# Kernel optimization log

Hardware: AMD Instinct MI355X
Metric: run time of the kernel (lower is better)

Reference implementation:

```python
import jax, jax.numpy as jnp
import numpy as np

D_MODEL = 512
NUM_HEADS = 8
WINDOW = 64
HEAD_DIM = D_MODEL // NUM_HEADS


def setup_inputs() -> dict:
    key = jax.random.key(0)
    k1, k2, k3 = jax.random.split(key, 3)
    B, F, L, D = 4, 16, 2048, D_MODEL
    x = jax.random.normal(k1, (B, F, L, D), dtype=jnp.float32)
    w_qkv = jax.random.normal(k2, (D, 3 * D), dtype=jnp.float32) * (1.0 / np.sqrt(D))
    b_qkv = jnp.zeros((3 * D,), dtype=jnp.float32)
    w_proj = jax.random.normal(k3, (D, D), dtype=jnp.float32) * (1.0 / np.sqrt(D))
    b_proj = jnp.zeros((D,), dtype=jnp.float32)
    return {"x": x, "w_qkv": w_qkv, "b_qkv": b_qkv, "w_proj": w_proj, "b_proj": b_proj}


def reference(x, w_qkv, b_qkv, w_proj, b_proj):
    B, F, L, D = x.shape
    W = WINDOW
    H, hd = NUM_HEADS, HEAD_DIM
    nw = L // W  # L chosen divisible by window_size; pad path is identity here
    # partition into windows: (B, F, nw, W, D)
    xw = x.reshape(B, F, nw, W, D)
    # fused QKV projection
    qkv = jnp.einsum('bfnwd,de->bfnwe', xw, w_qkv) + b_qkv  # (B,F,nw,W,3D)
    qkv = qkv.reshape(B, F, nw, W, 3, H, hd)
    q = qkv[..., 0, :, :]  # (B,F,nw,W,H,hd)
    k = qkv[..., 1, :, :]
    v = qkv[..., 2, :, :]
    scale = 1.0 / np.sqrt(hd).astype(np.float32)
    # per-window attention: scores (B,F,nw,H,W,W)
    scores = jnp.einsum('bfnqhd,bfnkhd->bfnhqk', q, k) * scale
    attn = jax.nn.softmax(scores, axis=-1)
    out = jnp.einsum('bfnhqk,bfnkhd->bfnqhd', attn, v)  # (B,F,nw,W,H,hd)
    out = out.reshape(B, F, nw, W, D)
    out = jnp.einsum('bfnwd,de->bfnwe', out, w_proj) + b_proj
    return out.reshape(B, F, L, D)
```

## Files before the change

### kernel.cpp

```cpp
#include <hip/hip_runtime.h>

typedef __attribute__((ext_vector_type(8))) short short8;
typedef __attribute__((ext_vector_type(4))) float f32x4;
typedef unsigned short u16;
typedef unsigned int u32;

__device__ __forceinline__ u16 f2bf(float f){
  union { float f; u32 u; } v; v.f = f;
  u32 u = v.u;
  u32 r = (u + 0x7FFFu + ((u >> 16) & 1u)) >> 16;
  return (u16)r;
}

__device__ __forceinline__ u32 cvtpk(float a, float b){
  u32 r;
  asm("v_cvt_pk_bf16_f32 %0, %1, %2" : "=v"(r) : "v"(a), "v"(b));
  return r;
}

__device__ __forceinline__ int swz(int row, int cb){ return cb ^ ((row & 7) << 4); }

__device__ __forceinline__ void gload16(const void* g, void* l){
  __builtin_amdgcn_global_load_lds(
      (const __attribute__((address_space(1))) unsigned int*)g,
      (__attribute__((address_space(3))) unsigned int*)l, 16, 0, 0);
}

__global__ void convert_weights_swz(const float* __restrict__ wqkv,
                                    const float* __restrict__ wproj,
                                    u16* __restrict__ wq_swz,
                                    u16* __restrict__ wpt){
  int c = blockIdx.x * 256 + threadIdx.x;
  union { u16 u[8]; uint4 v; } t;
  if (c < 98304){
    int tile = c >> 10, row = (c >> 3) & 127, c7 = c & 7;
    int bn = tile >> 3, kt = tile & 7;
    int j  = c7 ^ (row & 7);
    int e  = bn * 128 + row;
    int k0 = kt * 64 + j * 8;
    #pragma unroll
    for (int i = 0; i < 8; ++i) t.u[i] = f2bf(wqkv[(long)(k0 + i) * 1536 + e]);
    *reinterpret_cast<uint4*>(wq_swz + (long)c * 8) = t.v;
  } else {
    int t2 = c - 98304;
    int cc = t2 >> 6;
    int kc = (t2 & 63) << 3;
    #pragma unroll
    for (int i = 0; i < 8; ++i) t.u[i] = f2bf(wproj[(long)(kc + i) * 512 + cc]);
    *reinterpret_cast<uint4*>(wpt + (long)cc * 512 + kc) = t.v;
  }
}

__global__ void convert_x(const float* __restrict__ x, u16* __restrict__ xbf){
  int c = blockIdx.x * 256 + threadIdx.x;
  int tile = c >> 10, row = (c >> 3) & 127, c7 = c & 7;
  int bm = tile >> 3, kt = tile & 7;
  int j  = c7 ^ (row & 7);
  const float* src = x + (long)(bm * 128 + row) * 512 + kt * 64 + j * 8;
  float4 v0 = *reinterpret_cast<const float4*>(src);
  float4 v1 = *reinterpret_cast<const float4*>(src + 4);
  union { u16 u[8]; uint4 v; } t;
  t.u[0] = f2bf(v0.x); t.u[1] = f2bf(v0.y); t.u[2] = f2bf(v0.z); t.u[3] = f2bf(v0.w);
  t.u[4] = f2bf(v1.x); t.u[5] = f2bf(v1.y); t.u[6] = f2bf(v1.z); t.u[7] = f2bf(v1.w);
  *reinterpret_cast<uint4*>(xbf + (long)c * 8) = t.v;
}

__global__ __launch_bounds__(512, 2) void qkv_gemm256(
    const u16*  __restrict__ xbf,
    const u16*  __restrict__ wswz,
    const float* __restrict__ bqkv,
    u16* __restrict__ qkv)
{
  __shared__ char smem[131072];

  const int tid = threadIdx.x;
  const int l = tid & 63, w = tid >> 6;
  const int g = l >> 4,  ln = l & 15;
  const int wm = w >> 2, wn = w & 3;

  int hb   = blockIdx.x;
  int work = (hb & 7) * 384 + (hb >> 3);
  int bn   = work % 6;
  int bm   = work / 6;

  f32x4 acc[8][4];
  #pragma unroll
  for (int m = 0; m < 8; ++m)
    #pragma unroll
    for (int n = 0; n < 4; ++n) acc[m][n] = (f32x4){0.f,0.f,0.f,0.f};

  auto stage_slot = [&](int s){
    int kt = s >> 1, h = s & 1;
    char* base = smem + (s & 3) * 32768;
    const char* sa = (const char*)xbf  + ((long)(bm*2+h)*8 + kt)*16384;
    const char* sb = (const char*)wswz + ((long)(bn*2+h)*8 + kt)*16384;
    gload16(sa + (long)tid*16,         base + w*1024);
    gload16(sa + (long)(512+tid)*16,   base + 8192 + w*1024);
    gload16(sb + (long)tid*16,         base + 16384 + w*1024);
    gload16(sb + (long)(512+tid)*16,   base + 24576 + w*1024);
  };

  stage_slot(0); stage_slot(1); stage_slot(2); stage_slot(3);
  asm volatile("s_waitcnt vmcnt(8)" ::: "memory");
  __builtin_amdgcn_s_barrier();

  const int bro = (wn & 1) * 64;
  for (int t = 0; t < 8; ++t){
    const char* Abase = smem + ((2*t + wm) & 3) * 32768;
    const char* Bbase = smem + ((2*t + (wn >> 1)) & 3) * 32768 + 16384;
    short8 a[8][2], b[4][2];
    #pragma unroll
    for (int m = 0; m < 8; ++m){
      int r = m*16 + ln;
      #pragma unroll
      for (int ks = 0; ks < 2; ++ks)
        a[m][ks] = *reinterpret_cast<const short8*>(
            Abase + r*128 + (((ks*4 + g) ^ (r & 7)) << 4));
    }
    #pragma unroll
    for (int n = 0; n < 4; ++n){
      int r = bro + n*16 + ln;
      #pragma unroll
      for (int ks = 0; ks < 2; ++ks)
        b[n][ks] = *reinterpret_cast<const short8*>(
            Bbase + r*128 + (((ks*4 + g) ^ (r & 7)) << 4));
    }
    asm volatile("s_waitcnt lgkmcnt(0)" ::: "memory");
    __builtin_amdgcn_s_barrier();
    if (t < 6){ stage_slot(2*t + 4); stage_slot(2*t + 5); }
    __builtin_amdgcn_s_setprio(1);
    #pragma unroll
    for (int m = 0; m < 8; ++m)
      #pragma unroll
      for (int n = 0; n < 4; ++n)
        #pragma unroll
        for (int ks = 0; ks < 2; ++ks)
          acc[m][n] = __builtin_amdgcn_mfma_f32_16x16x32_bf16(
              a[m][ks], b[n][ks], acc[m][n], 0, 0, 0);
    __builtin_amdgcn_s_setprio(0);
    if (t < 6)       asm volatile("s_waitcnt vmcnt(8)" ::: "memory");
    else if (t == 6) asm volatile("s_waitcnt vmcnt(0)" ::: "memory");
    if (t < 7) __builtin_amdgcn_s_barrier();
  }

  u16* ldsC = (u16*)smem;
  #pragma unroll
  for (int ph = 0; ph < 2; ++ph){
    #pragma unroll
    for (int mf = 0; mf < 4; ++mf){
      int m = ph*4 + mf;
      #pragma unroll
      for (int n = 0; n < 4; ++n){
        int col = wn*64 + n*16 + ln;
        float bias = bqkv[bn*256 + col];
        int lr0 = wm*64 + mf*16 + g*4;
        #pragma unroll
        for (int r = 0; r < 4; ++r)
          ldsC[(lr0 + r)*264 + col] = f2bf(acc[m][n][r] + bias);
      }
    }
    __syncthreads();
    {
      int lr = tid >> 2, seg = tid & 3;
      const char* src = (const char*)(ldsC + lr*264) + seg*128;
      long gr = (long)bm*256 + (lr >> 6)*128 + ph*64 + (lr & 63);
      char* dst = (char*)qkv + (gr*1536 + bn*256)*2 + seg*128;
      #pragma unroll
      for (int j = 0; j < 8; ++j)
        *reinterpret_cast<uint4*>(dst + j*16) = *reinterpret_cast<const uint4*>(src + j*16);
    }
    __syncthreads();
  }
}

__global__ __launch_bounds__(512, 4) void winattn_proj(
    const u16* __restrict__ qkv,
    const u16* __restrict__ wpt,
    const float* __restrict__ bproj,
    float* __restrict__ out)
{
  __shared__ u16 lds[8][4096];
  const int tid = threadIdx.x;
  const int l = tid & 63, w = tid >> 6;
  const int g = l >> 4,  ln = l & 15;
  const int gh = g >> 1, gl = g & 1;
  const long tokb = (long)blockIdx.x * 64;
  u16* vt = lds[w];
  const int h = w;

  {
    const int dg = l & 3, tg = l >> 2;
    uint4 vr[4][2];
    #pragma unroll
    for (int r = 0; r < 4; ++r){
      const char* vrow = (const char*)(qkv + (tokb + tg*4 + r) * 1536 + 1024 + h*64 + dg*16);
      vr[r][0] = *reinterpret_cast<const uint4*>(vrow);
      vr[r][1] = *reinterpret_cast<const uint4*>(vrow + 16);
    }
    #pragma unroll
    for (int dd = 0; dd < 16; ++dd){
      int d = dg*16 + dd;
      int sub = dd & 7, hi = dd >> 3;
      uint2 pk;
      pk.x = (u32)((const u16*)&vr[0][hi])[sub] | ((u32)((const u16*)&vr[1][hi])[sub] << 16);
      pk.y = (u32)((const u16*)&vr[2][hi])[sub] | ((u32)((const u16*)&vr[3][hi])[sub] << 16);
      *reinterpret_cast<uint2*>((char*)vt + d*128 + swz(d, tg*8)) = pk;
    }
  }

  f32x4 oacc[4][4];
  #pragma unroll
  for (int m = 0; m < 4; ++m)
    #pragma unroll
    for (int n = 0; n < 4; ++n) oacc[m][n] = (f32x4){0.f,0.f,0.f,0.f};

  const int lnA = ln + 32*gl;

  #pragma unroll
  for (int half = 0; half < 2; ++half){
    short8 qa[2][2];
    #pragma unroll
    for (int j = 0; j < 2; ++j){
      const char* qrow = (const char*)(qkv + (tokb + (half*2+j)*16 + ln) * 1536 + h*64 + g*8);
      qa[j][0] = *reinterpret_cast<const short8*>(qrow);
      qa[j][1] = *reinterpret_cast<const short8*>(qrow + 64);
    }
    f32x4 st[4][2];
    #pragma unroll
    for (int mk = 0; mk < 4; ++mk){
      st[mk][0] = (f32x4){0.f,0.f,0.f,0.f};
      st[mk][1] = (f32x4){0.f,0.f,0.f,0.f};
    }
    #pragma unroll
    for (int mk = 0; mk < 4; ++mk){
      const char* krow = (const char*)(qkv + (tokb + mk*16 + ln) * 1536 + 512 + h*64 + g*8);
      short8 kb0 = *reinterpret_cast<const short8*>(krow);
      short8 kb1 = *reinterpret_cast<const short8*>(krow + 64);
      #pragma unroll
      for (int j = 0; j < 2; ++j){
        st[mk][j] = __builtin_amdgcn_mfma_f32_16x16x32_bf16(kb0, qa[j][0], st[mk][j], 0, 0, 0);
        st[mk][j] = __builtin_amdgcn_mfma_f32_16x16x32_bf16(kb1, qa[j][1], st[mk][j], 0, 0, 0);
      }
    }
    u32 warr[4][2][2];
    #pragma unroll
    for (int j = 0; j < 2; ++j){
      float mx = -3.4e38f;
      #pragma unroll
      for (int mk = 0; mk < 4; ++mk)
        #pragma unroll
        for (int r = 0; r < 4; ++r) mx = fmaxf(mx, st[mk][j][r]);
      mx = fmaxf(mx, __shfl_xor(mx, 16, 64));
      mx = fmaxf(mx, __shfl_xor(mx, 32, 64));
      float s = 0.f;
      #pragma unroll
      for (int mk = 0; mk < 4; ++mk)
        #pragma unroll
        for (int r = 0; r < 4; ++r){
          float p = __expf((st[mk][j][r] - mx) * 0.125f);
          st[mk][j][r] = p; s += p;
        }
      s += __shfl_xor(s, 16, 64);
      s += __shfl_xor(s, 32, 64);
      float inv = 1.f / s;
      #pragma unroll
      for (int mk = 0; mk < 4; ++mk){
        warr[mk][j][0] = cvtpk(st[mk][j][0]*inv, st[mk][j][1]*inv);
        warr[mk][j][1] = cvtpk(st[mk][j][2]*inv, st[mk][j][3]*inv);
      }
    }
    __builtin_amdgcn_s_setprio(1);
    #pragma unroll
    for (int ks = 0; ks < 2; ++ks){
      short8 vb[4];
      #pragma unroll
      for (int n = 0; n < 4; ++n){
        int row = n*16 + ln;
        vb[n] = *reinterpret_cast<const short8*>((char*)vt + row*128 + swz(row, (ks*32 + g*8)*2));
      }
      #pragma unroll
      for (int mo = 0; mo < 2; ++mo){
        int m = half*2 + mo;
        u32 c0a = warr[2*ks  ][mo][0], c0b = warr[2*ks  ][mo][1];
        u32 c1a = warr[2*ks+1][mo][0], c1b = warr[2*ks+1][mo][1];
        u32 s0a = (u32)__shfl((int)c0a, lnA, 64);
        u32 s1a = (u32)__shfl((int)c1a, lnA, 64);
        u32 s0b = (u32)__shfl((int)c0b, lnA, 64);
        u32 s1b = (u32)__shfl((int)c1b, lnA, 64);
        u32 t0a = (u32)__shfl((int)c0a, lnA+16, 64);
        u32 t1a = (u32)__shfl((int)c1a, lnA+16, 64);
        u32 t0b = (u32)__shfl((int)c0b, lnA+16, 64);
        u32 t1b = (u32)__shfl((int)c1b, lnA+16, 64);
        union { u32 u[4]; short8 v; } pf;
        pf.u[0] = gh ? s1a : s0a;
        pf.u[1] = gh ? s1b : s0b;
        pf.u[2] = gh ? t1a : t0a;
        pf.u[3] = gh ? t1b : t0b;
        #pragma unroll
        for (int n = 0; n < 4; ++n)
          oacc[m][n] = __builtin_amdgcn_mfma_f32_16x16x32_bf16(pf.v, vb[n], oacc[m][n], 0, 0, 0);
      }
    }
    __builtin_amdgcn_s_setprio(0);
  }

  #pragma unroll
  for (int m = 0; m < 4; ++m)
    #pragma unroll
    for (int n = 0; n < 4; ++n){
      int d = n*16 + ln;
      #pragma unroll
      for (int r = 0; r < 4; ++r){
        int t = m*16 + g*4 + r;
        *reinterpret_cast<u16*>((char*)vt + t*128 + swz(t, d*2)) = f2bf(oacc[m][n][r]);
      }
    }

  __syncthreads();

  f32x4 acc[4][4];
  #pragma unroll
  for (int m = 0; m < 4; ++m)
    #pragma unroll
    for (int n = 0; n < 4; ++n) acc[m][n] = (f32x4){0.f,0.f,0.f,0.f};

  for (int hh = 0; hh < 8; ++hh){
    const char* obuf = (const char*)lds[hh];
    #pragma unroll
    for (int ks = 0; ks < 2; ++ks){
      short8 a[4], b[4];
      #pragma unroll
      for (int m = 0; m < 4; ++m){
        int row = m*16 + ln;
        a[m] = *reinterpret_cast<const short8*>(obuf + row*128 + swz(row, (ks*32 + g*8)*2));
      }
      #pragma unroll
      for (int n = 0; n < 4; ++n){
        int e = w*64 + n*16 + ln;
        b[n] = *reinterpret_cast<const short8*>(wpt + (long)e*512 + hh*64 + ks*32 + g*8);
      }
      __builtin_amdgcn_s_setprio(1);
      #pragma unroll
      for (int m = 0; m < 4; ++m)
        #pragma unroll
        for (int n = 0; n < 4; ++n)
          acc[m][n] = __builtin_amdgcn_mfma_f32_16x16x32_bf16(a[m], b[n], acc[m][n], 0, 0, 0);
      __builtin_amdgcn_s_setprio(0);
    }
  }

  #pragma unroll
  for (int n = 0; n < 4; ++n){
    int col = w*64 + n*16 + ln;
    float bias = bproj[col];
    #pragma unroll
    for (int m = 0; m < 4; ++m){
      #pragma unroll
      for (int r = 0; r < 4; ++r){
        int t = m*16 + g*4 + r;
        out[(tokb + t) * 512 + col] = acc[m][n][r] + bias;
      }
    }
  }
}

__global__ void convert_weights(const float* __restrict__ wqkv,
                                const float* __restrict__ wproj,
                                u16* __restrict__ wqkvt,
                                u16* __restrict__ wprojt){
  int tid = blockIdx.x * 256 + threadIdx.x;
  union { u16 u[8]; uint4 v; } tmp;
  if (tid < 1536 * 64){
    int e  = tid >> 6;
    int kc = (tid & 63) << 3;
    #pragma unroll
    for (int i = 0; i < 8; ++i) tmp.u[i] = f2bf(wqkv[(long)(kc + i) * 1536 + e]);
    *reinterpret_cast<uint4*>(wqkvt + (long)e * 512 + kc) = tmp.v;
  } else {
    int t2 = tid - 1536 * 64;
    int c  = t2 >> 6;
    int kc = (t2 & 63) << 3;
    #pragma unroll
    for (int i = 0; i < 8; ++i) tmp.u[i] = f2bf(wproj[(long)(kc + i) * 512 + c]);
    *reinterpret_cast<uint4*>(wprojt + (long)c * 512 + kc) = tmp.v;
  }
}

__global__ __launch_bounds__(512, 2) void fused_winattn(
    const float* __restrict__ x,
    const u16*  __restrict__ wqkvt,
    const float* __restrict__ bqkv,
    const u16*  __restrict__ wprojt,
    const float* __restrict__ bproj,
    float* __restrict__ out)
{
  __shared__ u16 lds_x[64 * 512];
  __shared__ u16 lds_q[64 * 64];
  __shared__ u16 lds_k[64 * 64];
  __shared__ u16 lds_vt[64 * 64];
  __shared__ u16 lds_p[64 * 64];

  const int tid = threadIdx.x;
  const int l   = tid & 63;
  const int w   = tid >> 6;
  const int g   = l >> 4;
  const int ln  = l & 15;
  const long tokbase = (long)blockIdx.x * 64;

  {
    const float4* xv = reinterpret_cast<const float4*>(x + tokbase * 512);
    #pragma unroll
    for (int j = 0; j < 16; ++j){
      int i   = j * 512 + tid;
      int row = i >> 7;
      int c4  = i & 127;
      float4 v = xv[i];
      uint2 pk;
      pk.x = (u32)f2bf(v.x) | ((u32)f2bf(v.y) << 16);
      pk.y = (u32)f2bf(v.z) | ((u32)f2bf(v.w) << 16);
      int byte = row * 1024 + swz(row, c4 * 8);
      *reinterpret_cast<uint2*>(reinterpret_cast<char*>(lds_x) + byte) = pk;
    }
  }

  f32x4 oacc[4][4];
  #pragma unroll
  for (int m = 0; m < 4; ++m)
    #pragma unroll
    for (int n = 0; n < 4; ++n) oacc[m][n] = (f32x4){0.f, 0.f, 0.f, 0.f};

  const int mw   = w & 3;
  const int half = w >> 2;

  __syncthreads();

  for (int h = 0; h < 8; ++h){
    f32x4 qacc[6];
    #pragma unroll
    for (int j = 0; j < 6; ++j) qacc[j] = (f32x4){0.f, 0.f, 0.f, 0.f};
    int ebase[6];
    #pragma unroll
    for (int j = 0; j < 6; ++j){
      int nt = half * 6 + j;
      int sec = nt >> 2;
      ebase[j] = sec * 512 + h * 64 + (nt & 3) * 16;
    }
    const int arow = mw * 16 + ln;
    #pragma unroll
    for (int ks = 0; ks < 16; ++ks){
      short8 a = *reinterpret_cast<const short8*>(
          reinterpret_cast<const char*>(lds_x) + arow * 1024 + swz(arow, (ks * 32 + g * 8) * 2));
      #pragma unroll
      for (int j = 0; j < 6; ++j){
        short8 b = *reinterpret_cast<const short8*>(
            wqkvt + (long)(ebase[j] + ln) * 512 + ks * 32 + g * 8);
        qacc[j] = __builtin_amdgcn_mfma_f32_16x16x32_bf16(a, b, qacc[j], 0, 0, 0);
      }
    }
    #pragma unroll
    for (int j = 0; j < 6; ++j){
      int nt  = half * 6 + j;
      int sec = nt >> 2;
      float bias = bqkv[ebase[j] + ln];
      if (sec < 2){
        u16* dst = (sec == 0) ? lds_q : lds_k;
        int c = (nt & 3) * 16 + ln;
        #pragma unroll
        for (int r = 0; r < 4; ++r){
          int t = mw * 16 + g * 4 + r;
          int byte = t * 128 + swz(t, c * 2);
          *reinterpret_cast<u16*>(reinterpret_cast<char*>(dst) + byte) = f2bf(qacc[j][r] + bias);
        }
      } else {
        int d  = (nt & 3) * 16 + ln;
        int t0 = mw * 16 + g * 4;
        uint2 pk;
        pk.x = (u32)f2bf(qacc[j][0] + bias) | ((u32)f2bf(qacc[j][1] + bias) << 16);
        pk.y = (u32)f2bf(qacc[j][2] + bias) | ((u32)f2bf(qacc[j][3] + bias) << 16);
        int byte = d * 128 + swz(d, t0 * 2);
        *reinterpret_cast<uint2*>(reinterpret_cast<char*>(lds_vt) + byte) = pk;
      }
    }
    __syncthreads();

    if (w < 4){
      f32x4 sacc[4];
      #pragma unroll
      for (int jt = 0; jt < 4; ++jt) sacc[jt] = (f32x4){0.f, 0.f, 0.f, 0.f};
      #pragma unroll
      for (int ks = 0; ks < 2; ++ks){
        int qrow = w * 16 + ln;
        short8 a = *reinterpret_cast<const short8*>(
            reinterpret_cast<const char*>(lds_q) + qrow * 128 + swz(qrow, (ks * 32 + g * 8) * 2));
        #pragma unroll
        for (int jt = 0; jt < 4; ++jt){
          int krow = jt * 16 + ln;
          short8 b = *reinterpret_cast<const short8*>(
              reinterpret_cast<const char*>(lds_k) + krow * 128 + swz(krow, (ks * 32 + g * 8) * 2));
          sacc[jt] = __builtin_amdgcn_mfma_f32_16x16x32_bf16(a, b, sacc[jt], 0, 0, 0);
        }
      }
      #pragma unroll
      for (int r = 0; r < 4; ++r){
        float mx = fmaxf(fmaxf(sacc[0][r], sacc[1][r]), fmaxf(sacc[2][r], sacc[3][r]));
        mx = fmaxf(mx, __shfl_xor(mx, 1, 64));
        mx = fmaxf(mx, __shfl_xor(mx, 2, 64));
        mx = fmaxf(mx, __shfl_xor(mx, 4, 64));
        mx = fmaxf(mx, __shfl_xor(mx, 8, 64));
        float p[4], s = 0.f;
        #pragma unroll
        for (int jt = 0; jt < 4; ++jt){
          p[jt] = __expf((sacc[jt][r] - mx) * 0.125f);
          s += p[jt];
        }
        s += __shfl_xor(s, 1, 64);
        s += __shfl_xor(s, 2, 64);
        s += __shfl_xor(s, 4, 64);
        s += __shfl_xor(s, 8, 64);
        float inv = 1.f / s;
        int i = w * 16 + g * 4 + r;
        #pragma unroll
        for (int jt = 0; jt < 4; ++jt){
          int c = jt * 16 + ln;
          int byte = i * 128 + swz(i, c * 2);
          *reinterpret_cast<u16*>(reinterpret_cast<char*>(lds_p) + byte) = f2bf(p[jt] * inv);
        }
      }
    }
    __syncthreads();

    {
      int mc  = w & 3;
      int nc0 = (w >> 2) * 2;
      f32x4 oc[2];
      oc[0] = (f32x4){0.f, 0.f, 0.f, 0.f};
      oc[1] = (f32x4){0.f, 0.f, 0.f, 0.f};
      #pragma unroll
      for (int ks = 0; ks < 2; ++ks){
        int prow = mc * 16 + ln;
        short8 a = *reinterpret_cast<const short8*>(
            reinterpret_cast<const char*>(lds_p) + prow * 128 + swz(prow, (ks * 32 + g * 8) * 2));
        #pragma unroll
        for (int jj = 0; jj < 2; ++jj){
          int vrow = (nc0 + jj) * 16 + ln;
          short8 b = *reinterpret_cast<const short8*>(
              reinterpret_cast<const char*>(lds_vt) + vrow * 128 + swz(vrow, (ks * 32 + g * 8) * 2));
          oc[jj] = __builtin_amdgcn_mfma_f32_16x16x32_bf16(a, b, oc[jj], 0, 0, 0);
        }
      }
      #pragma unroll
      for (int jj = 0; jj < 2; ++jj){
        int d = (nc0 + jj) * 16 + ln;
        #pragma unroll
        for (int r = 0; r < 4; ++r){
          int t = mc * 16 + g * 4 + r;
          int byte = t * 128 + swz(t, d * 2);
          *reinterpret_cast<u16*>(reinterpret_cast<char*>(lds_q) + byte) = f2bf(oc[jj][r]);
        }
      }
    }
    __syncthreads();

    #pragma unroll
    for (int ks = 0; ks < 2; ++ks){
      short8 a[4];
      #pragma unroll
      for (int m = 0; m < 4; ++m){
        int row = m * 16 + ln;
        a[m] = *reinterpret_cast<const short8*>(
            reinterpret_cast<const char*>(lds_q) + row * 128 + swz(row, (ks * 32 + g * 8) * 2));
      }
      #pragma unroll
      for (int nt = 0; nt < 4; ++nt){
        int e = w * 64 + nt * 16 + ln;
        short8 b = *reinterpret_cast<const short8*>(
            wprojt + (long)e * 512 + h * 64 + ks * 32 + g * 8);
        #pragma unroll
        for (int m = 0; m < 4; ++m)
          oacc[m][nt] = __builtin_amdgcn_mfma_f32_16x16x32_bf16(a[m], b, oacc[m][nt], 0, 0, 0);
      }
    }
    __syncthreads();
  }

  #pragma unroll
  for (int nt = 0; nt < 4; ++nt){
    int col = w * 64 + nt * 16 + ln;
    float bias = bproj[col];
    #pragma unroll
    for (int m = 0; m < 4; ++m){
      #pragma unroll
      for (int r = 0; r < 4; ++r){
        int t = m * 16 + g * 4 + r;
        out[(tokbase + t) * 512 + col] = oacc[m][nt][r] + bias;
      }
    }
  }
}

extern "C" void kernel_launch(void* const* d_in, const int* in_sizes, int n_in,
                              void* d_out, int out_size, void* d_ws, size_t ws_size,
                              hipStream_t stream) {
  const float* x     = (const float*)d_in[0];
  const float* wqkv  = (const float*)d_in[1];
  const float* bqkv  = (const float*)d_in[2];
  const float* wproj = (const float*)d_in[3];
  const float* bproj = (const float*)d_in[4];
  float* out = (float*)d_out;

  const size_t NEED = 538968064ULL;
  if (ws_size >= NEED){
    u16* wq_swz = (u16*)d_ws;
    u16* wpt    = (u16*)((char*)d_ws + 1572864);
    u16* xbf    = (u16*)((char*)d_ws + 2097152);
    u16* qkv    = (u16*)((char*)d_ws + 136314880);
    convert_weights_swz<<<512, 256, 0, stream>>>(wqkv, wproj, wq_swz, wpt);
    convert_x<<<32768, 256, 0, stream>>>(x, xbf);
    qkv_gemm256<<<3072, 512, 0, stream>>>(xbf, wq_swz, bqkv, qkv);
    winattn_proj<<<2048, 512, 0, stream>>>(qkv, wpt, bproj, out);
  } else {
    u16* wqkvt  = (u16*)d_ws;
    u16* wprojt = wqkvt + 1536 * 512;
    convert_weights<<<512, 256, 0, stream>>>(wqkv, wproj, wqkvt, wprojt);
    fused_winattn<<<2048, 512, 0, stream>>>(x, wqkvt, bqkv, wprojt, bproj, out);
  }
}
```

Before: 663.8 us.

## Split QKV GEMM inner loop into interleaved LDS-read/MFMA phases; pre-tile proj weights

The QKV GEMM main loop now reads A and B fragments in halves and issues MFMAs in four quadrant phases separated by barriers and sched_barriers. The aim is to cut the live fragment registers (B shrinks from 4 to 2 fragments) and to overlap LDS reads with matrix math across waves, in a ping-pong style. Separately, the projection weights are stored in the exact fragment order the attention kernel loads, so each wave's global read of wproj is fully contiguous per lane. The extra barriers add synchronisation cost and could stall waves if the phases are poorly balanced.

```diff
diff --git a/kernel.cpp b/kernel.cpp
--- a/kernel.cpp
+++ b/kernel.cpp
@@ -26,10 +26,10 @@
       (__attribute__((address_space(3))) unsigned int*)l, 16, 0, 0);
 }
 
-__global__ void convert_weights_swz(const float* __restrict__ wqkv,
+__global__ void convert_weights_mix(const float* __restrict__ wqkv,
                                     const float* __restrict__ wproj,
                                     u16* __restrict__ wq_swz,
-                                    u16* __restrict__ wpt){
+                                    u16* __restrict__ wpf){
   int c = blockIdx.x * 256 + threadIdx.x;
   union { u16 u[8]; uint4 v; } t;
   if (c < 98304){
@@ -42,12 +42,19 @@
     for (int i = 0; i < 8; ++i) t.u[i] = f2bf(wqkv[(long)(k0 + i) * 1536 + e]);
     *reinterpret_cast<uint4*>(wq_swz + (long)c * 8) = t.v;
   } else {
-    int t2 = c - 98304;
-    int cc = t2 >> 6;
-    int kc = (t2 & 63) << 3;
-    #pragma unroll
-    for (int i = 0; i < 8; ++i) t.u[i] = f2bf(wproj[(long)(kc + i) * 512 + cc]);
-    *reinterpret_cast<uint4*>(wpt + (long)cc * 512 + kc) = t.v;
+    int c2 = c - 98304;
+    int cb = c2 >> 12;
+    int r  = c2 & 4095;
+    int hh = r >> 9;
+    int q  = r & 511;
+    int n  = q >> 7;
+    int ks = (q >> 6) & 1;
+    int l  = q & 63;
+    int e  = cb*64 + n*16 + (l & 15);
+    int k0 = hh*64 + ks*32 + (l >> 4)*8;
+    #pragma unroll
+    for (int i = 0; i < 8; ++i) t.u[i] = f2bf(wproj[(long)(k0 + i) * 512 + e]);
+    *reinterpret_cast<uint4*>(wpf + (long)c2 * 8) = t.v;
   }
 }
 
@@ -105,43 +112,72 @@
   __builtin_amdgcn_s_barrier();
 
   const int bro = (wn & 1) * 64;
+  short8 a[8][2], b[2][2];
+
   for (int t = 0; t < 8; ++t){
     const char* Abase = smem + ((2*t + wm) & 3) * 32768;
     const char* Bbase = smem + ((2*t + (wn >> 1)) & 3) * 32768 + 16384;
-    short8 a[8][2], b[4][2];
-    #pragma unroll
-    for (int m = 0; m < 8; ++m){
-      int r = m*16 + ln;
-      #pragma unroll
-      for (int ks = 0; ks < 2; ++ks)
-        a[m][ks] = *reinterpret_cast<const short8*>(
-            Abase + r*128 + (((ks*4 + g) ^ (r & 7)) << 4));
-    }
-    #pragma unroll
-    for (int n = 0; n < 4; ++n){
-      int r = bro + n*16 + ln;
-      #pragma unroll
-      for (int ks = 0; ks < 2; ++ks)
-        b[n][ks] = *reinterpret_cast<const short8*>(
-            Bbase + r*128 + (((ks*4 + g) ^ (r & 7)) << 4));
-    }
+
+    auto readA = [&](int mh){
+      #pragma unroll
+      for (int m = 0; m < 4; ++m){
+        int r = (mh*4 + m)*16 + ln;
+        #pragma unroll
+        for (int ks = 0; ks < 2; ++ks)
+          a[mh*4+m][ks] = *reinterpret_cast<const short8*>(
+              Abase + r*128 + (((ks*4 + g) ^ (r & 7)) << 4));
+      }
+    };
+    auto readB = [&](int nh){
+      #pragma unroll
+      for (int n = 0; n < 2; ++n){
+        int r = bro + (nh*2 + n)*16 + ln;
+        #pragma unroll
+        for (int ks = 0; ks < 2; ++ks)
+          b[n][ks] = *reinterpret_cast<const short8*>(
+              Bbase + r*128 + (((ks*4 + g) ^ (r & 7)) << 4));
+      }
+    };
+    auto mfma16 = [&](int mh, int nh){
+      __builtin_amdgcn_s_setprio(1);
+      #pragma unroll
+      for (int m = 0; m < 4; ++m)
+        #pragma unroll
+        for (int n = 0; n < 2; ++n)
+          #pragma unroll
+          for (int ks = 0; ks < 2; ++ks)
+            acc[mh*4+m][nh*2+n] = __builtin_amdgcn_mfma_f32_16x16x32_bf16(
+                a[mh*4+m][ks], b[n][ks], acc[mh*4+m][nh*2+n], 0, 0, 0);
+      __builtin_amdgcn_s_setprio(0);
+    };
+
+    readA(0); readB(0);
+    __builtin_amdgcn_s_barrier();
     asm volatile("s_waitcnt lgkmcnt(0)" ::: "memory");
+    __builtin_amdgcn_sched_barrier(0);
+    mfma16(0, 0);
+    __builtin_amdgcn_s_barrier();
+    readA(1);
+    __builtin_amdgcn_s_barrier();
+    asm volatile("s_waitcnt lgkmcnt(0)" ::: "memory");
+    __builtin_amdgcn_sched_barrier(0);
+    mfma16(1, 0);
+    __builtin_amdgcn_s_barrier();
+    readB(1);
+    __builtin_amdgcn_s_barrier();
+    asm volatile("s_waitcnt lgkmcnt(0)" ::: "memory");
+    __builtin_amdgcn_sched_barrier(0);
+    mfma16(0, 1);
     __builtin_amdgcn_s_barrier();
     if (t < 6){ stage_slot(2*t + 4); stage_slot(2*t + 5); }
-    __builtin_amdgcn_s_setprio(1);
-    #pragma unroll
-    for (int m = 0; m < 8; ++m)
-      #pragma unroll
-      for (int n = 0; n < 4; ++n)
-        #pragma unroll
-        for (int ks = 0; ks < 2; ++ks)
-          acc[m][n] = __builtin_amdgcn_mfma_f32_16x16x32_bf16(
-              a[m][ks], b[n][ks], acc[m][n], 0, 0, 0);
-    __builtin_amdgcn_s_setprio(0);
+    __builtin_amdgcn_s_barrier();
+    mfma16(1, 1);
     if (t < 6)       asm volatile("s_waitcnt vmcnt(8)" ::: "memory");
     else if (t == 6) asm volatile("s_waitcnt vmcnt(0)" ::: "memory");
     if (t < 7) __builtin_amdgcn_s_barrier();
   }
+
+  __syncthreads();
 
   u16* ldsC = (u16*)smem;
   #pragma unroll
@@ -175,7 +211,7 @@
 
 __global__ __launch_bounds__(512, 4) void winattn_proj(
     const u16* __restrict__ qkv,
-    const u16* __restrict__ wpt,
+    const u16* __restrict__ wpf,
     const float* __restrict__ bproj,
     float* __restrict__ out)
 {
@@ -335,10 +371,9 @@
         a[m] = *reinterpret_cast<const short8*>(obuf + row*128 + swz(row, (ks*32 + g*8)*2));
       }
       #pragma unroll
-      for (int n = 0; n < 4; ++n){
-        int e = w*64 + n*16 + ln;
-        b[n] = *reinterpret_cast<const short8*>(wpt + (long)e*512 + hh*64 + ks*32 + g*8);
-      }
+      for (int n = 0; n < 4; ++n)
+        b[n] = *reinterpret_cast<const short8*>(
+            wpf + ((((long)w*8 + hh)*4 + n)*2 + ks)*512 + (long)l*8);
       __builtin_amdgcn_s_setprio(1);
       #pragma unroll
       for (int m = 0; m < 4; ++m)
@@ -611,13 +646,13 @@
   const size_t NEED = 538968064ULL;
   if (ws_size >= NEED){
     u16* wq_swz = (u16*)d_ws;
-    u16* wpt    = (u16*)((char*)d_ws + 1572864);
+    u16* wpf    = (u16*)((char*)d_ws + 1572864);
     u16* xbf    = (u16*)((char*)d_ws + 2097152);
     u16* qkv    = (u16*)((char*)d_ws + 136314880);
-    convert_weights_swz<<<512, 256, 0, stream>>>(wqkv, wproj, wq_swz, wpt);
+    convert_weights_mix<<<512, 256, 0, stream>>>(wqkv, wproj, wq_swz, wpf);
     convert_x<<<32768, 256, 0, stream>>>(x, xbf);
     qkv_gemm256<<<3072, 512, 0, stream>>>(xbf, wq_swz, bqkv, qkv);
-    winattn_proj<<<2048, 512, 0, stream>>>(qkv, wpt, bproj, out);
+    winattn_proj<<<2048, 512, 0, stream>>>(qkv, wpf, bproj, out);
   } else {
     u16* wqkvt  = (u16*)d_ws;
     u16* wprojt = wqkvt + 1536 * 512;
```

New measurement: 617.3 us. 7.0% less time.
